# Performance work log

Hardware: AMD Instinct MI355X
Metric: run time of the kernel (lower is better)

Reference implementation:

```python
import jax, jax.numpy as jnp
import numpy as np

N_NODES = 100000
N_EDGES = 1600000
IN_DIM = 128
HEADS = 8
HEAD_DIM = 16  # output_dim 128 / heads 8
NEG_SLOPE = 0.2  # PyG GATConv default LeakyReLU slope


def setup_inputs() -> dict:
    key = jax.random.key(0)
    k1, k2, k3, k4, k5 = jax.random.split(key, 5)
    x = jax.random.normal(k1, (N_NODES, IN_DIM), dtype=jnp.float32)
    edge_index = jax.random.randint(k2, (2, N_EDGES), 0, N_NODES, dtype=jnp.int64)
    scale = 1.0 / np.sqrt(IN_DIM)
    W = jax.random.normal(k3, (IN_DIM, HEADS * HEAD_DIM), dtype=jnp.float32) * scale
    a_src = jax.random.normal(k4, (HEADS, HEAD_DIM), dtype=jnp.float32) * scale
    a_dst = jax.random.normal(k5, (HEADS, HEAD_DIM), dtype=jnp.float32) * scale
    bias = jnp.zeros((HEADS * HEAD_DIM,), dtype=jnp.float32)
    return {"x": x, "edge_index": edge_index, "W": W, "a_src": a_src, "a_dst": a_dst, "bias": bias}


def reference(x, edge_index, W, a_src, a_dst, bias):
    N = x.shape[0]
    H, D = a_src.shape
    # add self-loops (PyG GATConv default add_self_loops=True)
    loop = jnp.arange(N, dtype=edge_index.dtype)
    src = jnp.concatenate([edge_index[0], loop])  # message sources j
    dst = jnp.concatenate([edge_index[1], loop])  # message targets i

    h = (x @ W).reshape(N, H, D)  # per-head projected features
    alpha_src = jnp.sum(h * a_src, axis=-1)  # [N, H]
    alpha_dst = jnp.sum(h * a_dst, axis=-1)  # [N, H]

    # edge-wise attention logits, softmax over incoming edges of each dst node
    e = jax.nn.leaky_relu(alpha_src[src] + alpha_dst[dst], NEG_SLOPE)  # [E', H]
    e_max = jax.ops.segment_max(e, dst, num_segments=N)
    e_exp = jnp.exp(e - e_max[dst])
    denom = jax.ops.segment_sum(e_exp, dst, num_segments=N)
    alpha = e_exp / (denom[dst] + 1e-16)  # [E', H]

    # weighted scatter-sum of source features
    out = jax.ops.segment_sum(alpha[:, :, None] * h[src], dst, num_segments=N)  # [N, H, D]
    out = out.reshape(N, H * D) + bias
    # wrapper: ReLU (concat=True), dropout is identity in eval mode
    return jax.nn.relu(out)
```

## Files before the change

kernel.cpp:

```cpp
#include <hip/hip_runtime.h>
#include <hip/hip_bf16.h>

#define NEG_SLOPE 0.2f
#define NBUCK 782
#define ABLK 8192
#define CAP 3072

typedef __attribute__((ext_vector_type(8))) short bf16x8v;
typedef __attribute__((ext_vector_type(4))) float f32x4;

__device__ __forceinline__ unsigned f2bf_bits(float f) {
    unsigned u = __float_as_uint(f);
    return (u + 0x7fffu + ((u >> 16) & 1u)) >> 16;
}
__device__ __forceinline__ float bflo(unsigned u) { return __uint_as_float(u << 16); }
__device__ __forceinline__ float bfhi(unsigned u) { return __uint_as_float(u & 0xffff0000u); }

__global__ __launch_bounds__(256) void gemm_mfma(const float* __restrict__ x,
                                                 const short* __restrict__ WtE,
                                                 short* __restrict__ hout,
                                                 float* __restrict__ as,
                                                 float* __restrict__ ad, int N) {
    __shared__ short xs[64 * 136];
    __shared__ short wt[144 * 136];
    const int tid = threadIdx.x;
    const int r0 = blockIdx.x * 64;

#pragma unroll
    for (int p = 0; p < 9; ++p) {
        int idx = p * 256 + tid;
        int n = idx >> 4, kk = (idx & 15) * 8;
        *(uint4*)&wt[n * 136 + kk] = *(const uint4*)(WtE + n * 128 + kk);
    }
#pragma unroll
    for (int p = 0; p < 8; ++p) {
        int lin = p * 1024 + tid * 4;
        int row = lin >> 7, k = lin & 127;
        int gr = r0 + row;
        int grc = gr < N ? gr : N - 1;
        float4 v = *(const float4*)(x + (size_t)grc * 128 + k);
        unsigned p0 = f2bf_bits(v.x) | (f2bf_bits(v.y) << 16);
        unsigned p1 = f2bf_bits(v.z) | (f2bf_bits(v.w) << 16);
        *(uint2*)&xs[row * 136 + k] = make_uint2(p0, p1);
    }
    __syncthreads();

    const int wv = tid >> 6;
    const int lane = tid & 63;
    const int lc = lane & 15, quad = lane >> 4;
    f32x4 acc[9];
#pragma unroll
    for (int c = 0; c < 9; ++c) acc[c] = (f32x4){0.f, 0.f, 0.f, 0.f};
    const short* aB = &xs[(wv * 16 + lc) * 136 + quad * 8];
    const short* bB = &wt[lc * 136 + quad * 8];
#pragma unroll
    for (int kc = 0; kc < 4; ++kc) {
        bf16x8v af = *(const bf16x8v*)(aB + kc * 32);
#pragma unroll
        for (int c = 0; c < 9; ++c) {
            bf16x8v bf = *(const bf16x8v*)(bB + c * (16 * 136) + kc * 32);
            acc[c] = __builtin_amdgcn_mfma_f32_16x16x32_bf16(af, bf, acc[c], 0, 0, 0);
        }
    }

    const int rowb = r0 + wv * 16 + quad * 4;
#pragma unroll
    for (int c = 0; c < 8; ++c) {
#pragma unroll
        for (int r = 0; r < 4; ++r) {
            int row = rowb + r;
            if (row < N) hout[(size_t)row * 128 + c * 16 + lc] = (short)f2bf_bits(acc[c][r]);
        }
    }
#pragma unroll
    for (int r = 0; r < 4; ++r) {
        int row = rowb + r;
        if (row < N) {
            if (lc < 8) as[row * 8 + lc] = acc[8][r];
            else        ad[row * 8 + (lc - 8)] = acc[8][r];
        }
    }
}

__global__ __launch_bounds__(1024) void bucket_edges(const int* __restrict__ ei, int E,
                                                     int nblk,
                                                     unsigned* __restrict__ slab,
                                                     int2* __restrict__ csG,
                                                     const float* __restrict__ W,
                                                     const float* __restrict__ a_src,
                                                     const float* __restrict__ a_dst,
                                                     short* __restrict__ WtE) {
    const int t = threadIdx.x;
    const int blk = blockIdx.x;

    if (blk >= nblk) {
        int id = (blk - nblk) * 1024 + t;
        if (id < 144 * 128) {
            int n = id >> 7, k = id & 127;
            float v;
            if (n < 128) {
                v = W[k * 128 + n];
            } else if (n < 136) {
                int hh = n - 128; float s = 0.f;
#pragma unroll
                for (int d = 0; d < 16; ++d) s += W[k * 128 + hh * 16 + d] * a_src[hh * 16 + d];
                v = s;
            } else {
                int hh = n - 136; float s = 0.f;
#pragma unroll
                for (int d = 0; d < 16; ++d) s += W[k * 128 + hh * 16 + d] * a_dst[hh * 16 + d];
                v = s;
            }
            WtE[id] = (short)f2bf_bits(v);
        }
        return;
    }

    __shared__ int hist[1024];
    __shared__ int cur[NBUCK];
    __shared__ int wpart[16];
    const int base = blk * ABLK;
    int count = E - base; if (count > ABLK) count = ABLK;

    int sr[8], dr[8];
    hist[t] = 0;
#pragma unroll
    for (int k = 0; k < 8; ++k) {
        int i = k * 1024 + t;
        if (i < count) { sr[k] = ei[base + i]; dr[k] = ei[E + base + i]; }
    }
    __syncthreads();
#pragma unroll
    for (int k = 0; k < 8; ++k) {
        int i = k * 1024 + t;
        if (i < count) atomicAdd(&hist[dr[k] >> 7], 1);
    }
    __syncthreads();
    int v = hist[t];
    int lane = t & 63, wid = t >> 6;
    int sc = v;
#pragma unroll
    for (int off = 1; off < 64; off <<= 1) { int u = __shfl_up(sc, off); if (lane >= off) sc += u; }
    if (lane == 63) wpart[wid] = sc;
    __syncthreads();
    if (wid == 0 && lane < 16) {
        int wv = wpart[lane], wsum = wv;
#pragma unroll
        for (int off = 1; off < 16; off <<= 1) { int u = __shfl_up(wsum, off); if (lane >= off) wsum += u; }
        wpart[lane] = wsum - wv;
    }
    __syncthreads();
    int excl = sc - v + wpart[wid];
    if (t < NBUCK) {
        csG[(size_t)blk * NBUCK + t] = make_int2(v, excl);
        cur[t] = excl;
    }
    __syncthreads();
#pragma unroll
    for (int k = 0; k < 8; ++k) {
        int i = k * 1024 + t;
        if (i < count) {
            int d = dr[k];
            int pos = atomicAdd(&cur[d >> 7], 1);
            slab[(size_t)blk * ABLK + pos] = (unsigned)sr[k] | ((unsigned)(d & 127) << 17);
        }
    }
}

__global__ __launch_bounds__(512) void build_csr(const unsigned* __restrict__ slab,
                                                 const int2* __restrict__ csG,
                                                 int nblk, int N,
                                                 int* __restrict__ rowS,
                                                 int* __restrict__ rowE,
                                                 int* __restrict__ sortedSrc) {
    __shared__ int eL[CAP];
    __shared__ int incl[512];
    __shared__ int cS[512];
    __shared__ int stS[512];
    __shared__ int lp[128];
    __shared__ int wpart[8];
    __shared__ int halfSum;
    const int bb = blockIdx.x;
    const int t = threadIdx.x;
    const int nodeBase = bb << 7;
    const int bBase = bb * CAP;

    int c = 0, st = 0;
    if (t < nblk) { int2 cs = csG[(size_t)t * NBUCK + bb]; c = cs.x; st = cs.y; }
    cS[t] = c; stS[t] = st;
    if (t < 128) lp[t] = 0;
    int lane = t & 63, wid = t >> 6;
    int sc = c;
#pragma unroll
    for (int off = 1; off < 64; off <<= 1) { int u = __shfl_up(sc, off); if (lane >= off) sc += u; }
    if (lane == 63) wpart[wid] = sc;
    __syncthreads();
    if (wid == 0 && lane < 8) {
        int wv = wpart[lane], wsum = wv;
#pragma unroll
        for (int off = 1; off < 8; off <<= 1) { int u = __shfl_up(wsum, off); if (lane >= off) wsum += u; }
        wpart[lane] = wsum - wv;
    }
    __syncthreads();
    incl[t] = sc + wpart[wid];
    __syncthreads();
    int total = incl[511];
    if (total > CAP) total = CAP;
    {
        const int grp = t >> 3, li = t & 7;
        for (int s = grp; s < nblk; s += 64) {
            int cc = cS[s];
            int off0 = incl[s] - cc;
            const unsigned* p = slab + (size_t)s * ABLK + stS[s];
            for (int i = li; i < cc; i += 8) eL[off0 + i] = (int)p[i];
        }
    }
    __syncthreads();
    for (int e = t; e < total; e += 512) atomicAdd(&lp[((unsigned)eL[e]) >> 17], 1);
    __syncthreads();
    int cnt = 0, s2 = 0;
    if (t < 128) {
        cnt = lp[t];
        s2 = cnt;
#pragma unroll
        for (int off = 1; off < 64; off <<= 1) { int u = __shfl_up(s2, off); if (lane >= off) s2 += u; }
        if (t == 63) halfSum = s2;
    }
    __syncthreads();
    if (t < 128) {
        int inc2 = s2 + (t >= 64 ? halfSum : 0);
        int ex = inc2 - cnt;
        int gn = nodeBase + t;
        if (gn < N) { rowS[gn] = bBase + ex; rowE[gn] = bBase + ex + cnt; }
        lp[t] = ex;
    }
    __syncthreads();
    for (int e = t; e < total; e += 512) {
        unsigned pk = (unsigned)eL[e];
        int pos = atomicAdd(&lp[pk >> 17], 1);
        sortedSrc[bBase + pos] = (int)(pk & 0x1FFFFu);
    }
}

__global__ __launch_bounds__(256, 8) void aggregate(const int* __restrict__ rowS,
                                                    const int* __restrict__ rowE,
                                                    const int* __restrict__ sortedSrc,
                                                    const short* __restrict__ h,
                                                    const float* __restrict__ as,
                                                    const float* __restrict__ ad,
                                                    const float* __restrict__ bias,
                                                    float* __restrict__ out, int N) {
    const int lane = threadIdx.x & 63;
    const int wv = threadIdx.x >> 6;
    const int node = __builtin_amdgcn_readfirstlane(blockIdx.x * 4 + wv);
    if (node >= N) return;
    const int p = lane >> 3;
    const int start = __builtin_amdgcn_readfirstlane(rowS[node]);
    const int end   = __builtin_amdgcn_readfirstlane(rowE[node]);
    const float adv = ad[node * 8 + p];

    float accx = 0.f, accy = 0.f;
    float dsum = 0.f;

    int e = start;
    int iv = node;
    { int q = e + (lane & 7); if (q < end) iv = sortedSrc[q]; }

    while (e < end) {
        float asv[8]; unsigned hwv[8];
#pragma unroll
        for (int k = 0; k < 8; ++k) {
            int j = __builtin_amdgcn_readlane(iv, k);
            asv[k] = as[j * 8 + p];
            hwv[k] = *(const unsigned*)(h + (size_t)j * 128 + lane * 2);
        }
        int en = e + 8;
        int iv2 = node;
        { int q = en + (lane & 7); if (q < end) iv2 = sortedSrc[q]; }
#pragma unroll
        for (int k = 0; k < 8; ++k) {
            if (e + k < end) {
                float tt = asv[k] + adv;
                tt = tt > 0.f ? tt : NEG_SLOPE * tt;
                float w = __expf(tt);
                unsigned u = hwv[k];
                accx += w * bflo(u);
                accy += w * bfhi(u);
                dsum += w;
            }
        }
        iv = iv2; e = en;
    }

    {
        float tt = as[node * 8 + p] + adv;
        tt = tt > 0.f ? tt : NEG_SLOPE * tt;
        float w = __expf(tt);
        unsigned u = *(const unsigned*)(h + (size_t)node * 128 + lane * 2);
        accx += w * bflo(u);
        accy += w * bfhi(u);
        dsum += w;
    }

    float inv = 1.0f / (dsum + 1e-16f);
    float2 bv = *(const float2*)(bias + lane * 2);
    float o0 = accx * inv + bv.x;
    float o1 = accy * inv + bv.y;
    o0 = o0 > 0.f ? o0 : 0.f;
    o1 = o1 > 0.f ? o1 : 0.f;
    *(float2*)(out + (size_t)node * 128 + lane * 2) = make_float2(o0, o1);
}

extern "C" void kernel_launch(void* const* d_in, const int* in_sizes, int n_in,
                              void* d_out, int out_size, void* d_ws, size_t ws_size,
                              hipStream_t stream) {
    const float* x     = (const float*)d_in[0];
    const int*   ei    = (const int*)d_in[1];
    const float* W     = (const float*)d_in[2];
    const float* a_src = (const float*)d_in[3];
    const float* a_dst = (const float*)d_in[4];
    const float* bias  = (const float*)d_in[5];
    float* out = (float*)d_out;

    const int N = in_sizes[0] / 128;
    const int E = in_sizes[1] / 2;
    const int nblk = (E + ABLK - 1) / ABLK;

    char* ws = (char*)d_ws;
    size_t off = 0;
    auto alloc = [&](size_t bytes) { void* p = ws + off; off = (off + bytes + 255) & ~(size_t)255; return p; };
    short*    h         = (short*)alloc((size_t)N * 128 * 2);
    float*    as        = (float*)alloc((size_t)N * 8 * 4);
    float*    ad        = (float*)alloc((size_t)N * 8 * 4);
    unsigned* slab      = (unsigned*)alloc((size_t)nblk * ABLK * 4);
    int2*     csG       = (int2*)alloc((size_t)nblk * NBUCK * 8);
    int*      sortedSrc = (int*)alloc((size_t)NBUCK * CAP * 4);
    int*      rowS      = (int*)alloc((size_t)N * 4);
    int*      rowE      = (int*)alloc((size_t)N * 4);
    short*    WtE       = (short*)alloc((size_t)144 * 128 * 2);

    bucket_edges<<<nblk + 18, 1024, 0, stream>>>(ei, E, nblk, slab, csG, W, a_src, a_dst, WtE);
    gemm_mfma<<<(N + 63) / 64, 256, 0, stream>>>(x, WtE, h, as, ad, N);
    build_csr<<<NBUCK, 512, 0, stream>>>(slab, csG, nblk, N, rowS, rowE, sortedSrc);
    aggregate<<<(N + 3) / 4, 256, 0, stream>>>(rowS, rowE, sortedSrc, h, as, ad, bias, out, N);
}
```

Measured before the change: 222.9 us.

## Build CSR via global atomic degree count, scan, and scatter fused into GEMM

Replaces the two-pass bucketed sort (per-block shared-memory histograms, slab buffer, per-bucket CSR build) with a global-atomic degree count, a two-level prefix scan and an atomic scatter of source indices. The scatter blocks are appended to the GEMM launch so edge placement can overlap with the projection. This removes the slab round trip and the fixed per-bucket CAP layout. In exchange it adds more kernel launches and relies on contended global atomics and random-address writes.

```diff
diff --git a/kernel.cpp b/kernel.cpp
--- a/kernel.cpp
+++ b/kernel.cpp
@@ -2,9 +2,6 @@
 #include <hip/hip_bf16.h>
 
 #define NEG_SLOPE 0.2f
-#define NBUCK 782
-#define ABLK 8192
-#define CAP 3072
 
 typedef __attribute__((ext_vector_type(8))) short bf16x8v;
 typedef __attribute__((ext_vector_type(4))) float f32x4;
@@ -16,16 +13,127 @@
 __device__ __forceinline__ float bflo(unsigned u) { return __uint_as_float(u << 16); }
 __device__ __forceinline__ float bfhi(unsigned u) { return __uint_as_float(u & 0xffff0000u); }
 
-__global__ __launch_bounds__(256) void gemm_mfma(const float* __restrict__ x,
-                                                 const short* __restrict__ WtE,
-                                                 short* __restrict__ hout,
-                                                 float* __restrict__ as,
-                                                 float* __restrict__ ad, int N) {
+__global__ __launch_bounds__(256) void zero_deg(int* __restrict__ deg, int N) {
+    int i = blockIdx.x * 256 + threadIdx.x;
+    if (i < N) deg[i] = 0;
+}
+
+__global__ __launch_bounds__(256) void prep_count(const float* __restrict__ W,
+                                                  const float* __restrict__ a_src,
+                                                  const float* __restrict__ a_dst,
+                                                  short* __restrict__ WtE,
+                                                  const int* __restrict__ ei, int E,
+                                                  int* __restrict__ deg) {
+    const int t = threadIdx.x;
+    const int blk = blockIdx.x;
+    if (blk < 72) {
+        int id = blk * 256 + t;
+        int n = id >> 7, k = id & 127;
+        float v;
+        if (n < 128) {
+            v = W[k * 128 + n];
+        } else if (n < 136) {
+            int hh = n - 128; float s = 0.f;
+#pragma unroll
+            for (int d = 0; d < 16; ++d) s += W[k * 128 + hh * 16 + d] * a_src[hh * 16 + d];
+            v = s;
+        } else {
+            int hh = n - 136; float s = 0.f;
+#pragma unroll
+            for (int d = 0; d < 16; ++d) s += W[k * 128 + hh * 16 + d] * a_dst[hh * 16 + d];
+            v = s;
+        }
+        WtE[id] = (short)f2bf_bits(v);
+        return;
+    }
+    const int base = (blk - 72) * 1024;
+#pragma unroll
+    for (int k = 0; k < 4; ++k) {
+        int i = base + k * 256 + t;
+        if (i < E) atomicAdd(&deg[ei[E + i]], 1);
+    }
+}
+
+__global__ __launch_bounds__(1024) void scan1(const int* __restrict__ deg, int N,
+                                              int* __restrict__ rowS,
+                                              int* __restrict__ bsum) {
+    __shared__ int wpart[16];
+    const int t = threadIdx.x;
+    const int i = blockIdx.x * 1024 + t;
+    int d = (i < N) ? deg[i] : 0;
+    int lane = t & 63, wid = t >> 6;
+    int sc = d;
+#pragma unroll
+    for (int off = 1; off < 64; off <<= 1) { int u = __shfl_up(sc, off); if (lane >= off) sc += u; }
+    if (lane == 63) wpart[wid] = sc;
+    __syncthreads();
+    if (wid == 0 && lane < 16) {
+        int wv = wpart[lane], wsum = wv;
+#pragma unroll
+        for (int off = 1; off < 16; off <<= 1) { int u = __shfl_up(wsum, off); if (lane >= off) wsum += u; }
+        wpart[lane] = wsum - wv;
+    }
+    __syncthreads();
+    int excl = sc - d + wpart[wid];
+    if (i < N) rowS[i] = excl;
+    if (t == 1023) bsum[blockIdx.x] = excl + d;
+}
+
+__global__ __launch_bounds__(128) void scan2(int* __restrict__ bsum, int nb) {
+    __shared__ int w0;
+    const int t = threadIdx.x;
+    int v = (t < nb) ? bsum[t] : 0;
+    int lane = t & 63, wid = t >> 6;
+    int sc = v;
+#pragma unroll
+    for (int off = 1; off < 64; off <<= 1) { int u = __shfl_up(sc, off); if (lane >= off) sc += u; }
+    if (t == 63) w0 = sc;
+    __syncthreads();
+    int incl = sc + (wid ? w0 : 0);
+    if (t < nb) bsum[t] = incl - v;
+}
+
+__global__ __launch_bounds__(256) void fixup(const int* __restrict__ deg,
+                                             const int* __restrict__ boff, int N,
+                                             int* __restrict__ rowS,
+                                             int* __restrict__ rowE,
+                                             int* __restrict__ cur) {
+    int i = blockIdx.x * 256 + threadIdx.x;
+    if (i < N) {
+        int r = rowS[i] + boff[i >> 10];
+        rowS[i] = r;
+        rowE[i] = r + deg[i];
+        cur[i] = r;
+    }
+}
+
+__global__ __launch_bounds__(256) void gemm_scatter(const float* __restrict__ x,
+                                                    const short* __restrict__ WtE,
+                                                    short* __restrict__ hout,
+                                                    float* __restrict__ as,
+                                                    float* __restrict__ ad, int N, int gb,
+                                                    const int* __restrict__ ei, int E,
+                                                    int* __restrict__ cur,
+                                                    int* __restrict__ sortedSrc) {
     __shared__ short xs[64 * 136];
     __shared__ short wt[144 * 136];
     const int tid = threadIdx.x;
+
+    if (blockIdx.x >= gb) {
+        const int base = (blockIdx.x - gb) * 1024;
+#pragma unroll
+        for (int k = 0; k < 4; ++k) {
+            int i = base + k * 256 + tid;
+            if (i < E) {
+                int s = ei[i], d = ei[E + i];
+                int pos = atomicAdd(&cur[d], 1);
+                sortedSrc[pos] = s;
+            }
+        }
+        return;
+    }
+
     const int r0 = blockIdx.x * 64;
-
 #pragma unroll
     for (int p = 0; p < 9; ++p) {
         int idx = p * 256 + tid;
@@ -79,166 +187,6 @@
             if (lc < 8) as[row * 8 + lc] = acc[8][r];
             else        ad[row * 8 + (lc - 8)] = acc[8][r];
         }
-    }
-}
-
-__global__ __launch_bounds__(1024) void bucket_edges(const int* __restrict__ ei, int E,
-                                                     int nblk,
-                                                     unsigned* __restrict__ slab,
-                                                     int2* __restrict__ csG,
-                                                     const float* __restrict__ W,
-                                                     const float* __restrict__ a_src,
-                                                     const float* __restrict__ a_dst,
-                                                     short* __restrict__ WtE) {
-    const int t = threadIdx.x;
-    const int blk = blockIdx.x;
-
-    if (blk >= nblk) {
-        int id = (blk - nblk) * 1024 + t;
-        if (id < 144 * 128) {
-            int n = id >> 7, k = id & 127;
-            float v;
-            if (n < 128) {
-                v = W[k * 128 + n];
-            } else if (n < 136) {
-                int hh = n - 128; float s = 0.f;
-#pragma unroll
-                for (int d = 0; d < 16; ++d) s += W[k * 128 + hh * 16 + d] * a_src[hh * 16 + d];
-                v = s;
-            } else {
-                int hh = n - 136; float s = 0.f;
-#pragma unroll
-                for (int d = 0; d < 16; ++d) s += W[k * 128 + hh * 16 + d] * a_dst[hh * 16 + d];
-                v = s;
-            }
-            WtE[id] = (short)f2bf_bits(v);
-        }
-        return;
-    }
-
-    __shared__ int hist[1024];
-    __shared__ int cur[NBUCK];
-    __shared__ int wpart[16];
-    const int base = blk * ABLK;
-    int count = E - base; if (count > ABLK) count = ABLK;
-
-    int sr[8], dr[8];
-    hist[t] = 0;
-#pragma unroll
-    for (int k = 0; k < 8; ++k) {
-        int i = k * 1024 + t;
-        if (i < count) { sr[k] = ei[base + i]; dr[k] = ei[E + base + i]; }
-    }
-    __syncthreads();
-#pragma unroll
-    for (int k = 0; k < 8; ++k) {
-        int i = k * 1024 + t;
-        if (i < count) atomicAdd(&hist[dr[k] >> 7], 1);
-    }
-    __syncthreads();
-    int v = hist[t];
-    int lane = t & 63, wid = t >> 6;
-    int sc = v;
-#pragma unroll
-    for (int off = 1; off < 64; off <<= 1) { int u = __shfl_up(sc, off); if (lane >= off) sc += u; }
-    if (lane == 63) wpart[wid] = sc;
-    __syncthreads();
-    if (wid == 0 && lane < 16) {
-        int wv = wpart[lane], wsum = wv;
-#pragma unroll
-        for (int off = 1; off < 16; off <<= 1) { int u = __shfl_up(wsum, off); if (lane >= off) wsum += u; }
-        wpart[lane] = wsum - wv;
-    }
-    __syncthreads();
-    int excl = sc - v + wpart[wid];
-    if (t < NBUCK) {
-        csG[(size_t)blk * NBUCK + t] = make_int2(v, excl);
-        cur[t] = excl;
-    }
-    __syncthreads();
-#pragma unroll
-    for (int k = 0; k < 8; ++k) {
-        int i = k * 1024 + t;
-        if (i < count) {
-            int d = dr[k];
-            int pos = atomicAdd(&cur[d >> 7], 1);
-            slab[(size_t)blk * ABLK + pos] = (unsigned)sr[k] | ((unsigned)(d & 127) << 17);
-        }
-    }
-}
-
-__global__ __launch_bounds__(512) void build_csr(const unsigned* __restrict__ slab,
-                                                 const int2* __restrict__ csG,
-                                                 int nblk, int N,
-                                                 int* __restrict__ rowS,
-                                                 int* __restrict__ rowE,
-                                                 int* __restrict__ sortedSrc) {
-    __shared__ int eL[CAP];
-    __shared__ int incl[512];
-    __shared__ int cS[512];
-    __shared__ int stS[512];
-    __shared__ int lp[128];
-    __shared__ int wpart[8];
-    __shared__ int halfSum;
-    const int bb = blockIdx.x;
-    const int t = threadIdx.x;
-    const int nodeBase = bb << 7;
-    const int bBase = bb * CAP;
-
-    int c = 0, st = 0;
-    if (t < nblk) { int2 cs = csG[(size_t)t * NBUCK + bb]; c = cs.x; st = cs.y; }
-    cS[t] = c; stS[t] = st;
-    if (t < 128) lp[t] = 0;
-    int lane = t & 63, wid = t >> 6;
-    int sc = c;
-#pragma unroll
-    for (int off = 1; off < 64; off <<= 1) { int u = __shfl_up(sc, off); if (lane >= off) sc += u; }
-    if (lane == 63) wpart[wid] = sc;
-    __syncthreads();
-    if (wid == 0 && lane < 8) {
-        int wv = wpart[lane], wsum = wv;
-#pragma unroll
-        for (int off = 1; off < 8; off <<= 1) { int u = __shfl_up(wsum, off); if (lane >= off) wsum += u; }
-        wpart[lane] = wsum - wv;
-    }
-    __syncthreads();
-    incl[t] = sc + wpart[wid];
-    __syncthreads();
-    int total = incl[511];
-    if (total > CAP) total = CAP;
-    {
-        const int grp = t >> 3, li = t & 7;
-        for (int s = grp; s < nblk; s += 64) {
-            int cc = cS[s];
-            int off0 = incl[s] - cc;
-            const unsigned* p = slab + (size_t)s * ABLK + stS[s];
-            for (int i = li; i < cc; i += 8) eL[off0 + i] = (int)p[i];
-        }
-    }
-    __syncthreads();
-    for (int e = t; e < total; e += 512) atomicAdd(&lp[((unsigned)eL[e]) >> 17], 1);
-    __syncthreads();
-    int cnt = 0, s2 = 0;
-    if (t < 128) {
-        cnt = lp[t];
-        s2 = cnt;
-#pragma unroll
-        for (int off = 1; off < 64; off <<= 1) { int u = __shfl_up(s2, off); if (lane >= off) s2 += u; }
-        if (t == 63) halfSum = s2;
-    }
-    __syncthreads();
-    if (t < 128) {
-        int inc2 = s2 + (t >= 64 ? halfSum : 0);
-        int ex = inc2 - cnt;
-        int gn = nodeBase + t;
-        if (gn < N) { rowS[gn] = bBase + ex; rowE[gn] = bBase + ex + cnt; }
-        lp[t] = ex;
-    }
-    __syncthreads();
-    for (int e = t; e < total; e += 512) {
-        unsigned pk = (unsigned)eL[e];
-        int pos = atomicAdd(&lp[pk >> 17], 1);
-        sortedSrc[bBase + pos] = (int)(pk & 0x1FFFFu);
     }
 }
 
@@ -324,23 +272,29 @@
 
     const int N = in_sizes[0] / 128;
     const int E = in_sizes[1] / 2;
-    const int nblk = (E + ABLK - 1) / ABLK;
+    const int nEb = (E + 1023) / 1024;
+    const int gb  = (N + 63) / 64;
+    const int nb1 = (N + 1023) / 1024;
 
     char* ws = (char*)d_ws;
     size_t off = 0;
     auto alloc = [&](size_t bytes) { void* p = ws + off; off = (off + bytes + 255) & ~(size_t)255; return p; };
-    short*    h         = (short*)alloc((size_t)N * 128 * 2);
-    float*    as        = (float*)alloc((size_t)N * 8 * 4);
-    float*    ad        = (float*)alloc((size_t)N * 8 * 4);
-    unsigned* slab      = (unsigned*)alloc((size_t)nblk * ABLK * 4);
-    int2*     csG       = (int2*)alloc((size_t)nblk * NBUCK * 8);
-    int*      sortedSrc = (int*)alloc((size_t)NBUCK * CAP * 4);
-    int*      rowS      = (int*)alloc((size_t)N * 4);
-    int*      rowE      = (int*)alloc((size_t)N * 4);
-    short*    WtE       = (short*)alloc((size_t)144 * 128 * 2);
-
-    bucket_edges<<<nblk + 18, 1024, 0, stream>>>(ei, E, nblk, slab, csG, W, a_src, a_dst, WtE);
-    gemm_mfma<<<(N + 63) / 64, 256, 0, stream>>>(x, WtE, h, as, ad, N);
-    build_csr<<<NBUCK, 512, 0, stream>>>(slab, csG, nblk, N, rowS, rowE, sortedSrc);
+    short* h         = (short*)alloc((size_t)N * 128 * 2);
+    float* as        = (float*)alloc((size_t)N * 8 * 4);
+    float* ad        = (float*)alloc((size_t)N * 8 * 4);
+    int*   deg       = (int*)alloc((size_t)N * 4);
+    int*   rowS      = (int*)alloc((size_t)N * 4);
+    int*   rowE      = (int*)alloc((size_t)N * 4);
+    int*   cur       = (int*)alloc((size_t)N * 4);
+    int*   bsum      = (int*)alloc((size_t)128 * 4);
+    int*   sortedSrc = (int*)alloc((size_t)E * 4);
+    short* WtE       = (short*)alloc((size_t)144 * 128 * 2);
+
+    zero_deg<<<(N + 255) / 256, 256, 0, stream>>>(deg, N);
+    prep_count<<<72 + nEb, 256, 0, stream>>>(W, a_src, a_dst, WtE, ei, E, deg);
+    scan1<<<nb1, 1024, 0, stream>>>(deg, N, rowS, bsum);
+    scan2<<<1, 128, 0, stream>>>(bsum, nb1);
+    fixup<<<(N + 255) / 256, 256, 0, stream>>>(deg, bsum, N, rowS, rowE, cur);
+    gemm_scatter<<<gb + nEb, 256, 0, stream>>>(x, WtE, h, as, ad, N, gb, ei, E, cur, sortedSrc);
     aggregate<<<(N + 3) / 4, 256, 0, stream>>>(rowS, rowE, sortedSrc, h, as, ad, bias, out, N);
 }
```

Result: slower. 383.1 us (+71.9%).

## Fuse CSR build and aggregation into one kernel using shared-memory edge lists

Applied to the files above, without the earlier changes.

Merges build_csr and aggregate into a single kernel. Each block sorts its bucket of 128 destination nodes into shared memory, then its 8 waves aggregate those nodes straight from the LDS edge list. This drops the global writes and reads of sortedSrc/rowS/rowE and one kernel launch. In exchange, aggregation runs on only 782 blocks with larger LDS use, which cuts the parallelism and latency hiding available for the gather-heavy phase.

```diff
diff --git a/kernel.cpp b/kernel.cpp
--- a/kernel.cpp
+++ b/kernel.cpp
@@ -167,29 +167,33 @@
     }
 }
 
-__global__ __launch_bounds__(512) void build_csr(const unsigned* __restrict__ slab,
-                                                 const int2* __restrict__ csG,
-                                                 int nblk, int N,
-                                                 int* __restrict__ rowS,
-                                                 int* __restrict__ rowE,
-                                                 int* __restrict__ sortedSrc) {
+__global__ __launch_bounds__(512, 8) void csr_aggregate(const unsigned* __restrict__ slab,
+                                                        const int2* __restrict__ csG,
+                                                        int nblk, int N,
+                                                        const short* __restrict__ h,
+                                                        const float* __restrict__ as,
+                                                        const float* __restrict__ ad,
+                                                        const float* __restrict__ bias,
+                                                        float* __restrict__ out) {
     __shared__ int eL[CAP];
+    __shared__ int sEL[CAP];
     __shared__ int incl[512];
     __shared__ int cS[512];
     __shared__ int stS[512];
     __shared__ int lp[128];
+    __shared__ int lpS[128];
+    __shared__ int lpC[128];
     __shared__ int wpart[8];
     __shared__ int halfSum;
     const int bb = blockIdx.x;
     const int t = threadIdx.x;
     const int nodeBase = bb << 7;
-    const int bBase = bb * CAP;
+    const int lane = t & 63, wid = t >> 6;
 
     int c = 0, st = 0;
     if (t < nblk) { int2 cs = csG[(size_t)t * NBUCK + bb]; c = cs.x; st = cs.y; }
     cS[t] = c; stS[t] = st;
     if (t < 128) lp[t] = 0;
-    int lane = t & 63, wid = t >> 6;
     int sc = c;
 #pragma unroll
     for (int off = 1; off < 64; off <<= 1) { int u = __shfl_up(sc, off); if (lane >= off) sc += u; }
@@ -230,85 +234,77 @@
     if (t < 128) {
         int inc2 = s2 + (t >= 64 ? halfSum : 0);
         int ex = inc2 - cnt;
-        int gn = nodeBase + t;
-        if (gn < N) { rowS[gn] = bBase + ex; rowE[gn] = bBase + ex + cnt; }
+        lpS[t] = ex;
+        lpC[t] = cnt;
         lp[t] = ex;
     }
     __syncthreads();
     for (int e = t; e < total; e += 512) {
         unsigned pk = (unsigned)eL[e];
         int pos = atomicAdd(&lp[pk >> 17], 1);
-        sortedSrc[bBase + pos] = (int)(pk & 0x1FFFFu);
-    }
-}
-
-__global__ __launch_bounds__(256, 8) void aggregate(const int* __restrict__ rowS,
-                                                    const int* __restrict__ rowE,
-                                                    const int* __restrict__ sortedSrc,
-                                                    const short* __restrict__ h,
-                                                    const float* __restrict__ as,
-                                                    const float* __restrict__ ad,
-                                                    const float* __restrict__ bias,
-                                                    float* __restrict__ out, int N) {
-    const int lane = threadIdx.x & 63;
-    const int wv = threadIdx.x >> 6;
-    const int node = __builtin_amdgcn_readfirstlane(blockIdx.x * 4 + wv);
-    if (node >= N) return;
+        sEL[pos] = (int)(pk & 0x1FFFFu);
+    }
+    __syncthreads();
+
     const int p = lane >> 3;
-    const int start = __builtin_amdgcn_readfirstlane(rowS[node]);
-    const int end   = __builtin_amdgcn_readfirstlane(rowE[node]);
-    const float adv = ad[node * 8 + p];
-
-    float accx = 0.f, accy = 0.f;
-    float dsum = 0.f;
-
-    int e = start;
-    int iv = node;
-    { int q = e + (lane & 7); if (q < end) iv = sortedSrc[q]; }
-
-    while (e < end) {
-        float asv[8]; unsigned hwv[8];
-#pragma unroll
-        for (int k = 0; k < 8; ++k) {
-            int j = __builtin_amdgcn_readlane(iv, k);
-            asv[k] = as[j * 8 + p];
-            hwv[k] = *(const unsigned*)(h + (size_t)j * 128 + lane * 2);
-        }
-        int en = e + 8;
-        int iv2 = node;
-        { int q = en + (lane & 7); if (q < end) iv2 = sortedSrc[q]; }
-#pragma unroll
-        for (int k = 0; k < 8; ++k) {
-            if (e + k < end) {
-                float tt = asv[k] + adv;
-                tt = tt > 0.f ? tt : NEG_SLOPE * tt;
-                float w = __expf(tt);
-                unsigned u = hwv[k];
-                accx += w * bflo(u);
-                accy += w * bfhi(u);
-                dsum += w;
+    const int q7 = lane & 7;
+    for (int nl = wid; nl < 128; nl += 8) {
+        const int node = nodeBase + nl;
+        if (node >= N) continue;
+        const int start = __builtin_amdgcn_readfirstlane(lpS[nl]);
+        const int end   = start + __builtin_amdgcn_readfirstlane(lpC[nl]);
+        const float adv = ad[node * 8 + p];
+
+        float accx = 0.f, accy = 0.f, dsum = 0.f;
+
+        int e = start;
+        int iv = node;
+        { int q = e + q7; if (q < end) iv = sEL[q]; }
+
+        while (e < end) {
+            float asv[8]; unsigned hwv[8];
+#pragma unroll
+            for (int k = 0; k < 8; ++k) {
+                int j = __builtin_amdgcn_readlane(iv, k);
+                asv[k] = as[j * 8 + p];
+                hwv[k] = *(const unsigned*)(h + (size_t)j * 128 + lane * 2);
             }
-        }
-        iv = iv2; e = en;
-    }
-
-    {
-        float tt = as[node * 8 + p] + adv;
-        tt = tt > 0.f ? tt : NEG_SLOPE * tt;
-        float w = __expf(tt);
-        unsigned u = *(const unsigned*)(h + (size_t)node * 128 + lane * 2);
-        accx += w * bflo(u);
-        accy += w * bfhi(u);
-        dsum += w;
-    }
-
-    float inv = 1.0f / (dsum + 1e-16f);
-    float2 bv = *(const float2*)(bias + lane * 2);
-    float o0 = accx * inv + bv.x;
-    float o1 = accy * inv + bv.y;
-    o0 = o0 > 0.f ? o0 : 0.f;
-    o1 = o1 > 0.f ? o1 : 0.f;
-    *(float2*)(out + (size_t)node * 128 + lane * 2) = make_float2(o0, o1);
+            int en = e + 8;
+            int iv2 = node;
+            { int q = en + q7; if (q < end) iv2 = sEL[q]; }
+#pragma unroll
+            for (int k = 0; k < 8; ++k) {
+                if (e + k < end) {
+                    float tt = asv[k] + adv;
+                    tt = tt > 0.f ? tt : NEG_SLOPE * tt;
+                    float w = __expf(tt);
+                    unsigned u = hwv[k];
+                    accx += w * bflo(u);
+                    accy += w * bfhi(u);
+                    dsum += w;
+                }
+            }
+            iv = iv2; e = en;
+        }
+
+        {
+            float tt = as[node * 8 + p] + adv;
+            tt = tt > 0.f ? tt : NEG_SLOPE * tt;
+            float w = __expf(tt);
+            unsigned u = *(const unsigned*)(h + (size_t)node * 128 + lane * 2);
+            accx += w * bflo(u);
+            accy += w * bfhi(u);
+            dsum += w;
+        }
+
+        float inv = 1.0f / (dsum + 1e-16f);
+        float2 bv = *(const float2*)(bias + lane * 2);
+        float o0 = accx * inv + bv.x;
+        float o1 = accy * inv + bv.y;
+        o0 = o0 > 0.f ? o0 : 0.f;
+        o1 = o1 > 0.f ? o1 : 0.f;
+        *(float2*)(out + (size_t)node * 128 + lane * 2) = make_float2(o0, o1);
+    }
 }
 
 extern "C" void kernel_launch(void* const* d_in, const int* in_sizes, int n_in,
@@ -334,13 +330,9 @@
     float*    ad        = (float*)alloc((size_t)N * 8 * 4);
     unsigned* slab      = (unsigned*)alloc((size_t)nblk * ABLK * 4);
     int2*     csG       = (int2*)alloc((size_t)nblk * NBUCK * 8);
-    int*      sortedSrc = (int*)alloc((size_t)NBUCK * CAP * 4);
-    int*      rowS      = (int*)alloc((size_t)N * 4);
-    int*      rowE      = (int*)alloc((size_t)N * 4);
     short*    WtE       = (short*)alloc((size_t)144 * 128 * 2);
 
     bucket_edges<<<nblk + 18, 1024, 0, stream>>>(ei, E, nblk, slab, csG, W, a_src, a_dst, WtE);
     gemm_mfma<<<(N + 63) / 64, 256, 0, stream>>>(x, WtE, h, as, ad, N);
-    build_csr<<<NBUCK, 512, 0, stream>>>(slab, csG, nblk, N, rowS, rowE, sortedSrc);
-    aggregate<<<(N + 3) / 4, 256, 0, stream>>>(rowS, rowE, sortedSrc, h, as, ad, bias, out, N);
-}
+    csr_aggregate<<<NBUCK, 512, 0, stream>>>(slab, csG, nblk, N, h, as, ad, bias, out);
+}
```

Measured after the change: 230.7 us. +3.5%, slower.
